# Optimization experiments

Measured on AMD Instinct MI355X. Metric: run time of the kernel, lower is better.

The kernel has to match this reference:

```python
import jax, jax.numpy as jnp
import numpy as np

# 5-tap image-gradient filter (cross-correlation taps, as in F.conv2d)
_K5 = (-1.0 / 12.0, 2.0 / 3.0, 0.0, -2.0 / 3.0, 1.0 / 12.0)
ALPHA = BETA = GAMMA = DELTA = 1.0
MASK_COST = 1.0
ENTROPY_WEIGHT = 1.0


def _pen(x):
    return jnp.sqrt(x + 1e-5)


def _filt_w(x):
    # depthwise 1x5 filter along W, padding 2 (matches F.conv2d(x, kernel_gx, padding=(0,2)))
    W = x.shape[-1]
    xp = jnp.pad(x, ((0, 0), (0, 0), (0, 0), (2, 2)))
    out = _K5[0] * xp[..., 0:W]
    for j in range(1, 5):
        out = out + _K5[j] * xp[..., j:j + W]
    return out


def _filt_h(x):
    # depthwise 5x1 filter along H, padding 2
    H = x.shape[-2]
    xp = jnp.pad(x, ((0, 0), (0, 0), (2, 2), (0, 0)))
    out = _K5[0] * xp[..., 0:H, :]
    for j in range(1, 5):
        out = out + _K5[j] * xp[..., j:j + H, :]
    return out


def _warp(img, flow):
    # Bilinear warp: sample img at (x + flow_x, y + flow_y); out-of-range taps contribute 0
    B, C, H, W = img.shape
    xq = jnp.arange(W, dtype=img.dtype)[None, None, :] + flow[:, 0]  # (B,H,W)
    yq = jnp.arange(H, dtype=img.dtype)[None, :, None] + flow[:, 1]
    x0 = jnp.floor(xq)
    y0 = jnp.floor(yq)
    wx1 = xq - x0
    wy1 = yq - y0
    img_flat = img.reshape(B, C, H * W)

    def tap(xi, yi, w):
        valid = (xi >= 0) & (xi <= W - 1) & (yi >= 0) & (yi <= H - 1)
        xc = jnp.clip(xi, 0, W - 1).astype(jnp.int32)
        yc = jnp.clip(yi, 0, H - 1).astype(jnp.int32)
        idx = (yc * W + xc).reshape(B, 1, H * W)
        vals = jnp.take_along_axis(img_flat, jnp.broadcast_to(idx, (B, C, H * W)), axis=2)
        vals = vals.reshape(B, C, H, W)
        return vals * (w * valid.astype(img.dtype))[:, None]

    return (tap(x0, y0, (1 - wx1) * (1 - wy1)) + tap(x0 + 1, y0, wx1 * (1 - wy1))
            + tap(x0, y0 + 1, (1 - wx1) * wy1) + tap(x0 + 1, y0 + 1, wx1 * wy1))


def _border_mask(flow):
    B, _, H, W = flow.shape
    Xp = jnp.arange(W, dtype=flow.dtype)[None, None, :] + flow[:, 0]
    Yp = jnp.arange(H, dtype=flow.dtype)[None, :, None] + flow[:, 1]
    mask_x = jax.nn.sigmoid(Xp + 0.5) * (1.0 - jax.nn.sigmoid(Xp - (W - 0.5)))
    mask_y = jax.nn.sigmoid(Yp + 0.5) * (1.0 - jax.nn.sigmoid(Yp - (H - 0.5)))
    return mask_x * mask_y


def _direction_terms(flow_a, flow_b, img_a, img_b):
    # energy terms for one direction (warping *_b by flow_a)
    mask = _border_mask(flow_a)
    flow_b_warp = _warp(flow_b, flow_a)
    mag = jnp.sum(flow_a ** 2 + flow_b_warp ** 2, axis=1)
    diff = flow_a + flow_b_warp
    occ = 1.0 - jax.nn.sigmoid(jnp.sum(diff ** 2, axis=1) - (0.01 * mag + 0.5))
    mask = mask * occ
    mask_term = MASK_COST * jnp.sum(1.0 - mask, axis=(1, 2)).mean()
    img_b_warp = _warp(img_b, flow_a)
    A = jnp.sum((img_a - img_b_warp) ** 2, axis=1)
    data_term = ALPHA * jnp.sum(_pen(A) * mask, axis=(1, 2)).mean()
    dx = flow_a[..., 1:] - flow_a[..., :-1]
    dy = flow_a[:, :, 1:, :] - flow_a[:, :, :-1, :]
    Bt = (jnp.pad(jnp.sum(dx ** 2, axis=1), ((0, 0), (0, 0), (0, 1)))
          + jnp.pad(jnp.sum(dy ** 2, axis=1), ((0, 0), (0, 1), (0, 0))))
    smooth_term = BETA * jnp.sum(_pen(Bt), axis=(1, 2)).mean()
    Ct = (jnp.sum((_filt_w(img_a) - _filt_w(img_b_warp)) ** 2, axis=1)
          + jnp.sum((_filt_h(img_a) - _filt_h(img_b_warp)) ** 2, axis=1))
    grad_term = GAMMA * jnp.sum(_pen(Ct) * mask, axis=(1, 2)).mean()
    D = jnp.sum(diff ** 2, axis=1)
    fb_part = DELTA * jnp.sum(_pen(D) * mask, axis=(1, 2)).mean()
    return mask_term + data_term + smooth_term + grad_term + fb_part


def _elbo_epe(meanf, log_varf, meanb, log_varb, img1, img2, target, noise_f, noise_b):
    # reparameterized flow samples (Nsamples = 1)
    flowf = meanf + jnp.exp(log_varf / 2.0) * noise_f
    flowb = meanb + jnp.exp(log_varb / 2.0) * noise_b
    energy = (_direction_terms(flowf, flowb, img1, img2)
              + _direction_terms(flowb, flowf, img2, img1))
    entropy = (jnp.sum(log_varf, axis=(1, 2, 3)) / 2
               + jnp.sum(log_varb, axis=(1, 2, 3)) / 2).mean()
    elbo = energy - ENTROPY_WEIGHT * entropy
    epe = jnp.sqrt(jnp.sum((meanf - target) ** 2, axis=1)).mean()
    return elbo, epe


def setup_inputs() -> dict:
    key = jax.random.key(0)
    ks = jax.random.split(key, 9)
    B, H, W = 8, 384, 512
    return {
        "meanf": jax.random.normal(ks[0], (B, 2, H, W), jnp.float32),
        "log_varf": jax.random.normal(ks[1], (B, 2, H, W), jnp.float32),
        "meanb": jax.random.normal(ks[2], (B, 2, H, W), jnp.float32),
        "log_varb": jax.random.normal(ks[3], (B, 2, H, W), jnp.float32),
        "img1": jax.random.uniform(ks[4], (B, 3, H, W), jnp.float32),
        "img2": jax.random.uniform(ks[5], (B, 3, H, W), jnp.float32),
        "target": jax.random.normal(ks[6], (B, 2, H, W), jnp.float32),
        "noise_f": jax.random.normal(ks[7], (B, 2, H, W), jnp.float32),
        "noise_b": jax.random.normal(ks[8], (B, 2, H, W), jnp.float32),
    }


def reference(meanf, log_varf, meanb, log_varb, img1, img2, target, noise_f, noise_b):
    elbo, epe = _elbo_epe(meanf, log_varf, meanb, log_varb, img1, img2, target, noise_f, noise_b)
    return (elbo, epe)
```

## Files before the change

kernel.cpp:

```cpp
#include <hip/hip_runtime.h>
#include <math.h>

#define BATCH 8
#define IH 384
#define IW 512
#define NPIX (IH*IW)
#define BN (BATCH*NPIX)

#define TW 64
#define TH 16
#define RW (TW+4)
#define RH (TH+4)
#define RN (RW*RH)
#define NTX (IW/TW)
#define NTY (IH/TH)
#define NB_DIR (NTX*NTY*BATCH*2)

#define NB_FLOW 1536
#define ENT_OFF NB_DIR
#define EPE_OFF (ENT_OFF + NB_FLOW)
#define PART_FLOATS 8192

__device__ __forceinline__ float frcp_(float x){ return __builtin_amdgcn_rcpf(x); }
__device__ __forceinline__ float fsqrt_(float x){ return __builtin_amdgcn_sqrtf(x); }
__device__ __forceinline__ float sigmoidf_(float x){ return frcp_(1.0f + __expf(-x)); }

__device__ __forceinline__ float block_reduce_sum(float v){
    __shared__ float s[8];
    #pragma unroll
    for (int off=32; off>0; off>>=1) v += __shfl_down(v, off);
    int lane = threadIdx.x & 63, wid = threadIdx.x >> 6;
    if (lane==0) s[wid] = v;
    __syncthreads();
    float t = 0.f;
    if (wid==0){
        int nw = (blockDim.x+63)>>6;
        t = (lane < nw) ? s[lane] : 0.f;
        #pragma unroll
        for (int off=4; off>0; off>>=1) t += __shfl_down(t, off);
    }
    __syncthreads();
    return t;
}

__global__ __launch_bounds__(256)
void flows_kernel(const float* __restrict__ meanf, const float* __restrict__ log_varf,
                  const float* __restrict__ meanb, const float* __restrict__ log_varb,
                  const float* __restrict__ target,
                  const float* __restrict__ noise_f, const float* __restrict__ noise_b,
                  float* __restrict__ flowf, float* __restrict__ flowb,
                  float* __restrict__ part)
{
    int t = blockIdx.x*blockDim.x + threadIdx.x;
    const int NP4 = NPIX/4;
    int b = t / NP4, p4 = t - b*NP4;
    size_t i0 = ((size_t)b*2*NPIX)/4 + p4;
    size_t i1 = i0 + NPIX/4;

    const float4* mf = (const float4*)meanf;  const float4* lf = (const float4*)log_varf;
    const float4* mb = (const float4*)meanb;  const float4* lb = (const float4*)log_varb;
    const float4* nf = (const float4*)noise_f; const float4* nb = (const float4*)noise_b;
    const float4* tg = (const float4*)target;
    float4* ff = (float4*)flowf; float4* fbp = (float4*)flowb;

    float4 lf0 = lf[i0], lf1 = lf[i1], lb0 = lb[i0], lb1 = lb[i1];
    float4 mf0 = mf[i0], mf1 = mf[i1], mb0 = mb[i0], mb1 = mb[i1];
    float4 nf0 = nf[i0], nf1 = nf[i1], nb0 = nb[i0], nb1 = nb[i1];

    float4 o;
    o.x = mf0.x + __expf(0.5f*lf0.x)*nf0.x; o.y = mf0.y + __expf(0.5f*lf0.y)*nf0.y;
    o.z = mf0.z + __expf(0.5f*lf0.z)*nf0.z; o.w = mf0.w + __expf(0.5f*lf0.w)*nf0.w;
    ff[i0] = o;
    o.x = mf1.x + __expf(0.5f*lf1.x)*nf1.x; o.y = mf1.y + __expf(0.5f*lf1.y)*nf1.y;
    o.z = mf1.z + __expf(0.5f*lf1.z)*nf1.z; o.w = mf1.w + __expf(0.5f*lf1.w)*nf1.w;
    ff[i1] = o;
    o.x = mb0.x + __expf(0.5f*lb0.x)*nb0.x; o.y = mb0.y + __expf(0.5f*lb0.y)*nb0.y;
    o.z = mb0.z + __expf(0.5f*lb0.z)*nb0.z; o.w = mb0.w + __expf(0.5f*lb0.w)*nb0.w;
    fbp[i0] = o;
    o.x = mb1.x + __expf(0.5f*lb1.x)*nb1.x; o.y = mb1.y + __expf(0.5f*lb1.y)*nb1.y;
    o.z = mb1.z + __expf(0.5f*lb1.z)*nb1.z; o.w = mb1.w + __expf(0.5f*lb1.w)*nb1.w;
    fbp[i1] = o;

    float ent = (lf0.x+lf0.y+lf0.z+lf0.w) + (lf1.x+lf1.y+lf1.z+lf1.w)
              + (lb0.x+lb0.y+lb0.z+lb0.w) + (lb1.x+lb1.y+lb1.z+lb1.w);

    float4 t0 = tg[i0], t1 = tg[i1];
    float d0, d1, epe = 0.f;
    d0 = mf0.x - t0.x; d1 = mf1.x - t1.x; epe += fsqrt_(d0*d0 + d1*d1);
    d0 = mf0.y - t0.y; d1 = mf1.y - t1.y; epe += fsqrt_(d0*d0 + d1*d1);
    d0 = mf0.z - t0.z; d1 = mf1.z - t1.z; epe += fsqrt_(d0*d0 + d1*d1);
    d0 = mf0.w - t0.w; d1 = mf1.w - t1.w; epe += fsqrt_(d0*d0 + d1*d1);

    float s = block_reduce_sum(ent);
    if (threadIdx.x == 0) part[ENT_OFF + blockIdx.x] = s;
    float s2 = block_reduce_sum(epe);
    if (threadIdx.x == 0) part[EPE_OFF + blockIdx.x] = s2;
}

__global__ __launch_bounds__(256)
void dir_kernel(const float* __restrict__ flowf, const float* __restrict__ flowb,
                const float* __restrict__ img1, const float* __restrict__ img2,
                float* __restrict__ part)
{
    __shared__ float wlds[3][RH][RW];
    __shared__ float mlds[TH][TW];

    const int dir = blockIdx.z & 1, b = blockIdx.z >> 1;
    const float *pfa, *pfb, *pia, *pib;
    if (dir == 0){ pfa = flowf; pfb = flowb; pia = img1; pib = img2; }
    else         { pfa = flowb; pfb = flowf; pia = img2; pib = img1; }
    pfa += (size_t)b*2*NPIX; pfb += (size_t)b*2*NPIX;
    pia += (size_t)b*3*NPIX; pib += (size_t)b*3*NPIX;

    const int tw0 = blockIdx.x*TW, th0 = blockIdx.y*TH;
    const int tid = threadIdx.x;
    float local = 0.f;

    for (int i = tid; i < RN; i += 256){
        int hh = i / RW, ww = i - hh*RW;
        int gh = th0 + hh - 2, gw = tw0 + ww - 2;
        bool inimg = (gh >= 0) && (gh < IH) && (gw >= 0) && (gw < IW);
        float w0 = 0.f, w1 = 0.f, w2 = 0.f;
        if (inimg){
            int p = gh*IW + gw;
            float fax = pfa[p], fay = pfa[NPIX + p];
            float Xp = (float)gw + fax;
            float Yp = (float)gh + fay;

            float x0f = floorf(Xp), y0f = floorf(Yp);
            float wx1 = Xp - x0f, wy1 = Yp - y0f;
            float wx0 = 1.f - wx1, wy0 = 1.f - wy1;
            int idx[4]; float wt[4];
            {
                float xs[4] = {x0f, x0f + 1.f, x0f,       x0f + 1.f};
                float ys[4] = {y0f, y0f,       y0f + 1.f, y0f + 1.f};
                float wsx[4] = {wx0*wy0, wx1*wy0, wx0*wy1, wx1*wy1};
                #pragma unroll
                for (int k = 0; k < 4; ++k){
                    bool valid = (xs[k] >= 0.f) && (xs[k] <= (float)(IW-1)) &&
                                 (ys[k] >= 0.f) && (ys[k] <= (float)(IH-1));
                    float xc = fminf(fmaxf(xs[k], 0.f), (float)(IW-1));
                    float yc = fminf(fmaxf(ys[k], 0.f), (float)(IH-1));
                    idx[k] = (int)yc * IW + (int)xc;
                    wt[k]  = valid ? wsx[k] : 0.f;
                }
            }

            w0 = wt[0]*pib[idx[0]] + wt[1]*pib[idx[1]] + wt[2]*pib[idx[2]] + wt[3]*pib[idx[3]];
            {
                const float* s1 = pib + NPIX;
                const float* s2 = pib + 2*NPIX;
                w1 = wt[0]*s1[idx[0]] + wt[1]*s1[idx[1]] + wt[2]*s1[idx[2]] + wt[3]*s1[idx[3]];
                w2 = wt[0]*s2[idx[0]] + wt[1]*s2[idx[1]] + wt[2]*s2[idx[2]] + wt[3]*s2[idx[3]];
            }

            bool interior = (hh >= 2) && (hh < RH-2) && (ww >= 2) && (ww < RW-2);
            if (interior){
                float mx = sigmoidf_(Xp + 0.5f) * (1.f - sigmoidf_(Xp - ((float)IW - 0.5f)));
                float my = sigmoidf_(Yp + 0.5f) * (1.f - sigmoidf_(Yp - ((float)IH - 0.5f)));
                float bm = mx * my;

                float fbwx = wt[0]*pfb[idx[0]] + wt[1]*pfb[idx[1]] + wt[2]*pfb[idx[2]] + wt[3]*pfb[idx[3]];
                const float* pfb1 = pfb + NPIX;
                float fbwy = wt[0]*pfb1[idx[0]] + wt[1]*pfb1[idx[1]] + wt[2]*pfb1[idx[2]] + wt[3]*pfb1[idx[3]];

                float mag = fax*fax + fay*fay + fbwx*fbwx + fbwy*fbwy;
                float dfx = fax + fbwx, dfy = fay + fbwy;
                float D = dfx*dfx + dfy*dfy;
                float occ = 1.f - sigmoidf_(D - (0.01f*mag + 0.5f));
                float mask = bm * occ;
                mlds[hh-2][ww-2] = mask;

                local += (1.f - mask);

                float d0 = pia[p]        - w0;
                float d1 = pia[NPIX+p]   - w1;
                float d2 = pia[2*NPIX+p] - w2;
                local += fsqrt_(d0*d0 + d1*d1 + d2*d2 + 1e-5f) * mask;

                local += fsqrt_(D + 1e-5f) * mask;

                float Bt = 0.f;
                if (gw < IW-1){
                    float e0 = pfa[p+1] - fax;
                    float e1 = pfa[NPIX + p+1] - fay;
                    Bt += e0*e0 + e1*e1;
                }
                if (gh < IH-1){
                    float e0 = pfa[p+IW] - fax;
                    float e1 = pfa[NPIX + p+IW] - fay;
                    Bt += e0*e0 + e1*e1;
                }
                local += fsqrt_(Bt + 1e-5f);
            }
        }
        wlds[0][hh][ww] = w0;
        wlds[1][hh][ww] = w1;
        wlds[2][hh][ww] = w2;
    }
    __syncthreads();

    const float K0 = -1.f/12.f, K1 = 2.f/3.f, K3 = -2.f/3.f, K4 = 1.f/12.f;
    for (int i = tid; i < TW*TH; i += 256){
        int hh = i >> 6, ww = i & 63;
        int gh = th0 + hh, gw = tw0 + ww;
        int lh = hh + 2, lw = ww + 2;
        int p = gh*IW + gw;
        float Ct = 0.f;
        #pragma unroll
        for (int c = 0; c < 3; ++c){
            const float* A_ = pia + (size_t)c*NPIX;
            float gxa = 0.f;
            if (gw >= 2)    gxa += K0*A_[p-2];
            if (gw >= 1)    gxa += K1*A_[p-1];
            if (gw <= IW-2) gxa += K3*A_[p+1];
            if (gw <= IW-3) gxa += K4*A_[p+2];
            float gxw = K0*wlds[c][lh][lw-2] + K1*wlds[c][lh][lw-1]
                      + K3*wlds[c][lh][lw+1] + K4*wlds[c][lh][lw+2];
            float d = gxa - gxw; Ct += d*d;
            float gya = 0.f;
            if (gh >= 2)    gya += K0*A_[p-2*IW];
            if (gh >= 1)    gya += K1*A_[p-IW];
            if (gh <= IH-2) gya += K3*A_[p+IW];
            if (gh <= IH-3) gya += K4*A_[p+2*IW];
            float gyw = K0*wlds[c][lh-2][lw] + K1*wlds[c][lh-1][lw]
                      + K3*wlds[c][lh+1][lw] + K4*wlds[c][lh+2][lw];
            d = gya - gyw; Ct += d*d;
        }
        local += fsqrt_(Ct + 1e-5f) * mlds[hh][ww];
    }

    float s = block_reduce_sum(local);
    if (tid == 0) part[blockIdx.x + NTX*(blockIdx.y + NTY*blockIdx.z)] = s;
}

__global__ __launch_bounds__(256)
void finalize_kernel(const float* __restrict__ part, float* __restrict__ out)
{
    float e = 0.f, ent = 0.f, epe = 0.f;
    for (int i = threadIdx.x; i < NB_DIR; i += 256) e += part[i];
    for (int i = threadIdx.x; i < NB_FLOW; i += 256){
        ent += part[ENT_OFF + i];
        epe += part[EPE_OFF + i];
    }
    e   = block_reduce_sum(e);
    ent = block_reduce_sum(ent);
    epe = block_reduce_sum(epe);
    if (threadIdx.x == 0){
        out[0] = e / (float)BATCH - ent / (2.f * (float)BATCH);
        out[1] = epe / ((float)BATCH * (float)NPIX);
    }
}

extern "C" void kernel_launch(void* const* d_in, const int* in_sizes, int n_in,
                              void* d_out, int out_size, void* d_ws, size_t ws_size,
                              hipStream_t stream)
{
    const float* meanf    = (const float*)d_in[0];
    const float* log_varf = (const float*)d_in[1];
    const float* meanb    = (const float*)d_in[2];
    const float* log_varb = (const float*)d_in[3];
    const float* img1     = (const float*)d_in[4];
    const float* img2     = (const float*)d_in[5];
    const float* target   = (const float*)d_in[6];
    const float* noise_f  = (const float*)d_in[7];
    const float* noise_b  = (const float*)d_in[8];

    float* ws    = (float*)d_ws;
    float* part  = ws;
    float* flowf = ws + PART_FLOATS;
    float* flowb = flowf + 2*(size_t)BN;

    const int threads = 256;

    flows_kernel<<<NB_FLOW, threads, 0, stream>>>(meanf, log_varf, meanb, log_varb,
                                                  target, noise_f, noise_b,
                                                  flowf, flowb, part);

    dim3 grid(NTX, NTY, BATCH*2);
    dir_kernel<<<grid, threads, 0, stream>>>(flowf, flowb, img1, img2, part);

    finalize_kernel<<<1, threads, 0, stream>>>(part, (float*)d_out);
}
```

Baseline: 264.2 us.

## Interleave flows as float2 and images as padded float4 for vector gathers

Adds a repack kernel that turns the planar 3-channel images into interleaved float4 pixels, and makes the flow kernel write flows as interleaved float2. The direction kernel then fetches each bilinear tap with one vector load instead of three (image) or two (flow) scalar gathers, and keeps the warped image in LDS as float4. This cuts the number of scattered memory transactions in the warp and gradient stages. The cost is an extra pass over both images, about a third more image bytes from the zero padding, and more workspace memory.

```diff
diff --git a/kernel.cpp b/kernel.cpp
--- a/kernel.cpp
+++ b/kernel.cpp
@@ -17,6 +17,7 @@
 #define NB_DIR (NTX*NTY*BATCH*2)
 
 #define NB_FLOW 1536
+#define NB_IMG4 1536
 #define ENT_OFF NB_DIR
 #define EPE_OFF (ENT_OFF + NB_FLOW)
 #define PART_FLOATS 8192
@@ -44,42 +45,66 @@
 }
 
 __global__ __launch_bounds__(256)
+void repack_kernel(const float* __restrict__ img1, const float* __restrict__ img2,
+                   float4* __restrict__ img4_1, float4* __restrict__ img4_2)
+{
+    const float* src = blockIdx.z ? img2 : img1;
+    float4* dst      = blockIdx.z ? img4_2 : img4_1;
+    int t = blockIdx.x*blockDim.x + threadIdx.x;
+    const int NP4 = NPIX/4;
+    int b = t / NP4, p4 = t - b*NP4;
+    const float4* s = (const float4*)(src + (size_t)b*3*NPIX);
+    float4 c0 = s[p4], c1 = s[NP4 + p4], c2 = s[2*NP4 + p4];
+    float4* d = dst + (size_t)b*NPIX + 4*(size_t)p4;
+    d[0] = make_float4(c0.x, c1.x, c2.x, 0.f);
+    d[1] = make_float4(c0.y, c1.y, c2.y, 0.f);
+    d[2] = make_float4(c0.z, c1.z, c2.z, 0.f);
+    d[3] = make_float4(c0.w, c1.w, c2.w, 0.f);
+}
+
+__global__ __launch_bounds__(256)
 void flows_kernel(const float* __restrict__ meanf, const float* __restrict__ log_varf,
                   const float* __restrict__ meanb, const float* __restrict__ log_varb,
                   const float* __restrict__ target,
                   const float* __restrict__ noise_f, const float* __restrict__ noise_b,
-                  float* __restrict__ flowf, float* __restrict__ flowb,
+                  float2* __restrict__ flowf2, float2* __restrict__ flowb2,
                   float* __restrict__ part)
 {
     int t = blockIdx.x*blockDim.x + threadIdx.x;
     const int NP4 = NPIX/4;
     int b = t / NP4, p4 = t - b*NP4;
     size_t i0 = ((size_t)b*2*NPIX)/4 + p4;
-    size_t i1 = i0 + NPIX/4;
+    size_t i1 = i0 + NP4;
 
     const float4* mf = (const float4*)meanf;  const float4* lf = (const float4*)log_varf;
     const float4* mb = (const float4*)meanb;  const float4* lb = (const float4*)log_varb;
     const float4* nf = (const float4*)noise_f; const float4* nb = (const float4*)noise_b;
     const float4* tg = (const float4*)target;
-    float4* ff = (float4*)flowf; float4* fbp = (float4*)flowb;
 
     float4 lf0 = lf[i0], lf1 = lf[i1], lb0 = lb[i0], lb1 = lb[i1];
     float4 mf0 = mf[i0], mf1 = mf[i1], mb0 = mb[i0], mb1 = mb[i1];
     float4 nf0 = nf[i0], nf1 = nf[i1], nb0 = nb[i0], nb1 = nb[i1];
 
-    float4 o;
-    o.x = mf0.x + __expf(0.5f*lf0.x)*nf0.x; o.y = mf0.y + __expf(0.5f*lf0.y)*nf0.y;
-    o.z = mf0.z + __expf(0.5f*lf0.z)*nf0.z; o.w = mf0.w + __expf(0.5f*lf0.w)*nf0.w;
-    ff[i0] = o;
-    o.x = mf1.x + __expf(0.5f*lf1.x)*nf1.x; o.y = mf1.y + __expf(0.5f*lf1.y)*nf1.y;
-    o.z = mf1.z + __expf(0.5f*lf1.z)*nf1.z; o.w = mf1.w + __expf(0.5f*lf1.w)*nf1.w;
-    ff[i1] = o;
-    o.x = mb0.x + __expf(0.5f*lb0.x)*nb0.x; o.y = mb0.y + __expf(0.5f*lb0.y)*nb0.y;
-    o.z = mb0.z + __expf(0.5f*lb0.z)*nb0.z; o.w = mb0.w + __expf(0.5f*lb0.w)*nb0.w;
-    fbp[i0] = o;
-    o.x = mb1.x + __expf(0.5f*lb1.x)*nb1.x; o.y = mb1.y + __expf(0.5f*lb1.y)*nb1.y;
-    o.z = mb1.z + __expf(0.5f*lb1.z)*nb1.z; o.w = mb1.w + __expf(0.5f*lb1.w)*nb1.w;
-    fbp[i1] = o;
+    float4 fx, fy;
+    fx.x = mf0.x + __expf(0.5f*lf0.x)*nf0.x; fx.y = mf0.y + __expf(0.5f*lf0.y)*nf0.y;
+    fx.z = mf0.z + __expf(0.5f*lf0.z)*nf0.z; fx.w = mf0.w + __expf(0.5f*lf0.w)*nf0.w;
+    fy.x = mf1.x + __expf(0.5f*lf1.x)*nf1.x; fy.y = mf1.y + __expf(0.5f*lf1.y)*nf1.y;
+    fy.z = mf1.z + __expf(0.5f*lf1.z)*nf1.z; fy.w = mf1.w + __expf(0.5f*lf1.w)*nf1.w;
+    float2* df = flowf2 + (size_t)b*NPIX + 4*(size_t)p4;
+    df[0] = make_float2(fx.x, fy.x);
+    df[1] = make_float2(fx.y, fy.y);
+    df[2] = make_float2(fx.z, fy.z);
+    df[3] = make_float2(fx.w, fy.w);
+
+    fx.x = mb0.x + __expf(0.5f*lb0.x)*nb0.x; fx.y = mb0.y + __expf(0.5f*lb0.y)*nb0.y;
+    fx.z = mb0.z + __expf(0.5f*lb0.z)*nb0.z; fx.w = mb0.w + __expf(0.5f*lb0.w)*nb0.w;
+    fy.x = mb1.x + __expf(0.5f*lb1.x)*nb1.x; fy.y = mb1.y + __expf(0.5f*lb1.y)*nb1.y;
+    fy.z = mb1.z + __expf(0.5f*lb1.z)*nb1.z; fy.w = mb1.w + __expf(0.5f*lb1.w)*nb1.w;
+    float2* db = flowb2 + (size_t)b*NPIX + 4*(size_t)p4;
+    db[0] = make_float2(fx.x, fy.x);
+    db[1] = make_float2(fx.y, fy.y);
+    db[2] = make_float2(fx.z, fy.z);
+    db[3] = make_float2(fx.w, fy.w);
 
     float ent = (lf0.x+lf0.y+lf0.z+lf0.w) + (lf1.x+lf1.y+lf1.z+lf1.w)
               + (lb0.x+lb0.y+lb0.z+lb0.w) + (lb1.x+lb1.y+lb1.z+lb1.w);
@@ -98,19 +123,19 @@
 }
 
 __global__ __launch_bounds__(256)
-void dir_kernel(const float* __restrict__ flowf, const float* __restrict__ flowb,
-                const float* __restrict__ img1, const float* __restrict__ img2,
+void dir_kernel(const float2* __restrict__ flowf2, const float2* __restrict__ flowb2,
+                const float4* __restrict__ img4_1, const float4* __restrict__ img4_2,
                 float* __restrict__ part)
 {
-    __shared__ float wlds[3][RH][RW];
-    __shared__ float mlds[TH][TW];
+    __shared__ float4 wlds[RH][RW];
+    __shared__ float  mlds[TH][TW];
 
     const int dir = blockIdx.z & 1, b = blockIdx.z >> 1;
-    const float *pfa, *pfb, *pia, *pib;
-    if (dir == 0){ pfa = flowf; pfb = flowb; pia = img1; pib = img2; }
-    else         { pfa = flowb; pfb = flowf; pia = img2; pib = img1; }
-    pfa += (size_t)b*2*NPIX; pfb += (size_t)b*2*NPIX;
-    pia += (size_t)b*3*NPIX; pib += (size_t)b*3*NPIX;
+    const float2 *pfa, *pfb; const float4 *pia, *pib;
+    if (dir == 0){ pfa = flowf2; pfb = flowb2; pia = img4_1; pib = img4_2; }
+    else         { pfa = flowb2; pfb = flowf2; pia = img4_2; pib = img4_1; }
+    pfa += (size_t)b*NPIX; pfb += (size_t)b*NPIX;
+    pia += (size_t)b*NPIX; pib += (size_t)b*NPIX;
 
     const int tw0 = blockIdx.x*TW, th0 = blockIdx.y*TH;
     const int tid = threadIdx.x;
@@ -120,12 +145,12 @@
         int hh = i / RW, ww = i - hh*RW;
         int gh = th0 + hh - 2, gw = tw0 + ww - 2;
         bool inimg = (gh >= 0) && (gh < IH) && (gw >= 0) && (gw < IW);
-        float w0 = 0.f, w1 = 0.f, w2 = 0.f;
+        float4 wv = make_float4(0.f, 0.f, 0.f, 0.f);
         if (inimg){
             int p = gh*IW + gw;
-            float fax = pfa[p], fay = pfa[NPIX + p];
-            float Xp = (float)gw + fax;
-            float Yp = (float)gh + fay;
+            float2 fa = pfa[p];
+            float Xp = (float)gw + fa.x;
+            float Yp = (float)gh + fa.y;
 
             float x0f = floorf(Xp), y0f = floorf(Yp);
             float wx1 = Xp - x0f, wy1 = Yp - y0f;
@@ -146,13 +171,10 @@
                 }
             }
 
-            w0 = wt[0]*pib[idx[0]] + wt[1]*pib[idx[1]] + wt[2]*pib[idx[2]] + wt[3]*pib[idx[3]];
-            {
-                const float* s1 = pib + NPIX;
-                const float* s2 = pib + 2*NPIX;
-                w1 = wt[0]*s1[idx[0]] + wt[1]*s1[idx[1]] + wt[2]*s1[idx[2]] + wt[3]*s1[idx[3]];
-                w2 = wt[0]*s2[idx[0]] + wt[1]*s2[idx[1]] + wt[2]*s2[idx[2]] + wt[3]*s2[idx[3]];
-            }
+            float4 t0 = pib[idx[0]], t1 = pib[idx[1]], t2 = pib[idx[2]], t3 = pib[idx[3]];
+            wv.x = wt[0]*t0.x + wt[1]*t1.x + wt[2]*t2.x + wt[3]*t3.x;
+            wv.y = wt[0]*t0.y + wt[1]*t1.y + wt[2]*t2.y + wt[3]*t3.y;
+            wv.z = wt[0]*t0.z + wt[1]*t1.z + wt[2]*t2.z + wt[3]*t3.z;
 
             bool interior = (hh >= 2) && (hh < RH-2) && (ww >= 2) && (ww < RW-2);
             if (interior){
@@ -160,12 +182,12 @@
                 float my = sigmoidf_(Yp + 0.5f) * (1.f - sigmoidf_(Yp - ((float)IH - 0.5f)));
                 float bm = mx * my;
 
-                float fbwx = wt[0]*pfb[idx[0]] + wt[1]*pfb[idx[1]] + wt[2]*pfb[idx[2]] + wt[3]*pfb[idx[3]];
-                const float* pfb1 = pfb + NPIX;
-                float fbwy = wt[0]*pfb1[idx[0]] + wt[1]*pfb1[idx[1]] + wt[2]*pfb1[idx[2]] + wt[3]*pfb1[idx[3]];
-
-                float mag = fax*fax + fay*fay + fbwx*fbwx + fbwy*fbwy;
-                float dfx = fax + fbwx, dfy = fay + fbwy;
+                float2 f0 = pfb[idx[0]], f1 = pfb[idx[1]], f2 = pfb[idx[2]], f3 = pfb[idx[3]];
+                float fbwx = wt[0]*f0.x + wt[1]*f1.x + wt[2]*f2.x + wt[3]*f3.x;
+                float fbwy = wt[0]*f0.y + wt[1]*f1.y + wt[2]*f2.y + wt[3]*f3.y;
+
+                float mag = fa.x*fa.x + fa.y*fa.y + fbwx*fbwx + fbwy*fbwy;
+                float dfx = fa.x + fbwx, dfy = fa.y + fbwy;
                 float D = dfx*dfx + dfy*dfy;
                 float occ = 1.f - sigmoidf_(D - (0.01f*mag + 0.5f));
                 float mask = bm * occ;
@@ -173,59 +195,67 @@
 
                 local += (1.f - mask);
 
-                float d0 = pia[p]        - w0;
-                float d1 = pia[NPIX+p]   - w1;
-                float d2 = pia[2*NPIX+p] - w2;
+                float4 ia = pia[p];
+                float d0 = ia.x - wv.x, d1 = ia.y - wv.y, d2 = ia.z - wv.z;
                 local += fsqrt_(d0*d0 + d1*d1 + d2*d2 + 1e-5f) * mask;
 
                 local += fsqrt_(D + 1e-5f) * mask;
 
                 float Bt = 0.f;
                 if (gw < IW-1){
-                    float e0 = pfa[p+1] - fax;
-                    float e1 = pfa[NPIX + p+1] - fay;
+                    float2 r = pfa[p+1];
+                    float e0 = r.x - fa.x, e1 = r.y - fa.y;
                     Bt += e0*e0 + e1*e1;
                 }
                 if (gh < IH-1){
-                    float e0 = pfa[p+IW] - fax;
-                    float e1 = pfa[NPIX + p+IW] - fay;
+                    float2 d = pfa[p+IW];
+                    float e0 = d.x - fa.x, e1 = d.y - fa.y;
                     Bt += e0*e0 + e1*e1;
                 }
                 local += fsqrt_(Bt + 1e-5f);
             }
         }
-        wlds[0][hh][ww] = w0;
-        wlds[1][hh][ww] = w1;
-        wlds[2][hh][ww] = w2;
+        wlds[hh][ww] = wv;
     }
     __syncthreads();
 
     const float K0 = -1.f/12.f, K1 = 2.f/3.f, K3 = -2.f/3.f, K4 = 1.f/12.f;
+    const float4 Z = make_float4(0.f,0.f,0.f,0.f);
     for (int i = tid; i < TW*TH; i += 256){
         int hh = i >> 6, ww = i & 63;
         int gh = th0 + hh, gw = tw0 + ww;
         int lh = hh + 2, lw = ww + 2;
         int p = gh*IW + gw;
+
+        float4 axm2 = (gw >= 2)    ? pia[p-2]    : Z;
+        float4 axm1 = (gw >= 1)    ? pia[p-1]    : Z;
+        float4 axp1 = (gw <= IW-2) ? pia[p+1]    : Z;
+        float4 axp2 = (gw <= IW-3) ? pia[p+2]    : Z;
+        float4 aym2 = (gh >= 2)    ? pia[p-2*IW] : Z;
+        float4 aym1 = (gh >= 1)    ? pia[p-IW]   : Z;
+        float4 ayp1 = (gh <= IH-2) ? pia[p+IW]   : Z;
+        float4 ayp2 = (gh <= IH-3) ? pia[p+2*IW] : Z;
+
+        float4 wxm2 = wlds[lh][lw-2], wxm1 = wlds[lh][lw-1];
+        float4 wxp1 = wlds[lh][lw+1], wxp2 = wlds[lh][lw+2];
+        float4 wym2 = wlds[lh-2][lw], wym1 = wlds[lh-1][lw];
+        float4 wyp1 = wlds[lh+1][lw], wyp2 = wlds[lh+2][lw];
+
         float Ct = 0.f;
-        #pragma unroll
-        for (int c = 0; c < 3; ++c){
-            const float* A_ = pia + (size_t)c*NPIX;
-            float gxa = 0.f;
-            if (gw >= 2)    gxa += K0*A_[p-2];
-            if (gw >= 1)    gxa += K1*A_[p-1];
-            if (gw <= IW-2) gxa += K3*A_[p+1];
-            if (gw <= IW-3) gxa += K4*A_[p+2];
-            float gxw = K0*wlds[c][lh][lw-2] + K1*wlds[c][lh][lw-1]
-                      + K3*wlds[c][lh][lw+1] + K4*wlds[c][lh][lw+2];
-            float d = gxa - gxw; Ct += d*d;
-            float gya = 0.f;
-            if (gh >= 2)    gya += K0*A_[p-2*IW];
-            if (gh >= 1)    gya += K1*A_[p-IW];
-            if (gh <= IH-2) gya += K3*A_[p+IW];
-            if (gh <= IH-3) gya += K4*A_[p+2*IW];
-            float gyw = K0*wlds[c][lh-2][lw] + K1*wlds[c][lh-1][lw]
-                      + K3*wlds[c][lh+1][lw] + K4*wlds[c][lh+2][lw];
-            d = gya - gyw; Ct += d*d;
+        {
+            float d;
+            d = (K0*axm2.x + K1*axm1.x + K3*axp1.x + K4*axp2.x)
+              - (K0*wxm2.x + K1*wxm1.x + K3*wxp1.x + K4*wxp2.x); Ct += d*d;
+            d = (K0*axm2.y + K1*axm1.y + K3*axp1.y + K4*axp2.y)
+              - (K0*wxm2.y + K1*wxm1.y + K3*wxp1.y + K4*wxp2.y); Ct += d*d;
+            d = (K0*axm2.z + K1*axm1.z + K3*axp1.z + K4*axp2.z)
+              - (K0*wxm2.z + K1*wxm1.z + K3*wxp1.z + K4*wxp2.z); Ct += d*d;
+            d = (K0*aym2.x + K1*aym1.x + K3*ayp1.x + K4*ayp2.x)
+              - (K0*wym2.x + K1*wym1.x + K3*wyp1.x + K4*wyp2.x); Ct += d*d;
+            d = (K0*aym2.y + K1*aym1.y + K3*ayp1.y + K4*ayp2.y)
+              - (K0*wym2.y + K1*wym1.y + K3*wyp1.y + K4*wyp2.y); Ct += d*d;
+            d = (K0*aym2.z + K1*aym1.z + K3*ayp1.z + K4*ayp2.z)
+              - (K0*wym2.z + K1*wym1.z + K3*wyp1.z + K4*wyp2.z); Ct += d*d;
         }
         local += fsqrt_(Ct + 1e-5f) * mlds[hh][ww];
     }
@@ -266,19 +296,22 @@
     const float* noise_f  = (const float*)d_in[7];
     const float* noise_b  = (const float*)d_in[8];
 
-    float* ws    = (float*)d_ws;
-    float* part  = ws;
-    float* flowf = ws + PART_FLOATS;
-    float* flowb = flowf + 2*(size_t)BN;
+    float*  ws     = (float*)d_ws;
+    float*  part   = ws;
+    float2* flowf2 = (float2*)(ws + PART_FLOATS);
+    float2* flowb2 = flowf2 + (size_t)BN;
+    float4* img4_1 = (float4*)(flowb2 + (size_t)BN);
+    float4* img4_2 = img4_1 + (size_t)BN;
 
     const int threads = 256;
 
+    repack_kernel<<<dim3(NB_IMG4,1,2), threads, 0, stream>>>(img1, img2, img4_1, img4_2);
     flows_kernel<<<NB_FLOW, threads, 0, stream>>>(meanf, log_varf, meanb, log_varb,
                                                   target, noise_f, noise_b,
-                                                  flowf, flowb, part);
+                                                  flowf2, flowb2, part);
 
     dim3 grid(NTX, NTY, BATCH*2);
-    dir_kernel<<<grid, threads, 0, stream>>>(flowf, flowb, img1, img2, part);
+    dir_kernel<<<grid, threads, 0, stream>>>(flowf2, flowb2, img4_1, img4_2, part);
 
     finalize_kernel<<<1, threads, 0, stream>>>(part, (float*)d_out);
 }
```

New measurement: 286.1 us. 1.08x slower.
